# Kernel optimization log

Measured on AMD Instinct MI355X. Metric: run time of the kernel, lower is better.

Reference implementation:

```python
import jax, jax.numpy as jnp
import numpy as np

B, LQ, LK = 4, 2048, 2048
DQ, DK, DO = 1024, 1024, 1024


def setup_inputs() -> dict:
    key = jax.random.key(0)
    ks = jax.random.split(key, 9)
    s = 0.02
    return {
        "query_input": jax.random.normal(ks[0], (B, LQ, DQ), jnp.float32),
        "key_input": jax.random.normal(ks[1], (B, LK, DK), jnp.float32),
        "value_input": jax.random.normal(ks[2], (B, LK, DK), jnp.float32),
        "Wq": jax.random.normal(ks[3], (DQ, DO), jnp.float32) * s,
        "bq": jax.random.normal(ks[4], (DO,), jnp.float32) * s,
        "Wk": jax.random.normal(ks[5], (DK, DO), jnp.float32) * s,
        "bk": jax.random.normal(ks[6], (DO,), jnp.float32) * s,
        "Wv": jax.random.normal(ks[7], (DK, DO), jnp.float32) * s,
        "bv": jax.random.normal(ks[8], (DO,), jnp.float32) * s,
    }


def reference(query_input, key_input, value_input, Wq, bq, Wk, bk, Wv, bv):
    scale = jnp.asarray(DO, query_input.dtype) ** 0.5
    q = query_input @ Wq + bq              # [B, Lq, D]
    k = key_input @ Wk + bk                # [B, Lk, D]
    v = value_input @ Wv + bv              # [B, Lk, D]
    attn = jnp.einsum("bqd,bkd->bqk", q, k) / scale
    attn = jax.nn.softmax(attn, axis=-1)
    return jnp.einsum("bqk,bkd->bqd", attn, v)
```

## Files before the change

kernel.cpp:

```cpp
#include <hip/hip_runtime.h>

typedef _Float16 f16x8 __attribute__((ext_vector_type(8)));
typedef _Float16 f16x4 __attribute__((ext_vector_type(4)));
typedef float f32x4 __attribute__((ext_vector_type(4)));

__device__ __forceinline__ void lds_load16(const _Float16* g, _Float16* l) {
    __builtin_amdgcn_global_load_lds(
        (const __attribute__((address_space(1))) void*)g,
        (__attribute__((address_space(3))) void*)l,
        16, 0, 0);
}

template <int MODE>
__global__ __launch_bounds__(256, 2)
void gemm_core(const _Float16* A0, const _Float16* B0, void* C0, const float* b0,
               const _Float16* A1, const _Float16* B1, void* C1, const float* b1,
               const _Float16* A2, const _Float16* B2, void* C2, const float* b2,
               float* rowsum)
{
    constexpr int K   = (MODE == 5) ? 2048 : 1024;
    constexpr int LDA = (MODE == 5) ? 2048 : 1024;
    constexpr int LDB = (MODE == 5) ? 8192 : 1024;

    const int z = blockIdx.z;
    const int bx = blockIdx.x, by = blockIdx.y;

    __shared__ __align__(16) _Float16 As[2][256 * 32];
    __shared__ __align__(16) _Float16 Bs[2][128 * 32];

    const int t    = threadIdx.x;
    const int w    = t >> 6;
    const int lane = t & 63;
    const int ln   = lane & 15;
    const int kq   = lane >> 4;
    const int wm   = (w & 1) * 128;
    const int wn   = (w >> 1) * 64;

    const _Float16* A;
    const _Float16* B;
    size_t cbase = 0;
    int m0, n0;

    if (MODE == 0) {
        A = z == 0 ? A0 : z == 1 ? A1 : A2;
        B = z == 0 ? B0 : z == 1 ? B1 : B2;
        if (z == 2) { m0 = (by & 3) * 256; n0 = ((by >> 2) * 8 + bx) * 128; }
        else        { m0 = by * 256;       n0 = bx * 128; }
    } else if (MODE == 3) {
        A = A0 + (size_t)z * 2048 * 1024;
        B = B0 + (size_t)z * 2048 * 1024;
        cbase = (size_t)z * 2048 * 2048;
        rowsum += z * 2048;
        m0 = (by >> 1) * 256;
        n0 = ((by & 1) * 8 + bx) * 128;
    } else {
        A = A0 + (size_t)z * 2048 * 2048;
        B = B0 + (size_t)z * 2048;
        cbase = (size_t)z * 2048 * 1024;
        rowsum += z * 2048;
        m0 = by * 256;
        n0 = bx * 128;
    }

    const int r4 = t >> 2;
    const int sc = ((t & 3) ^ ((t >> 3) & 3)) * 8;
    const _Float16* gA = A + (size_t)(m0 + r4) * LDA + sc;
    const _Float16* gB = B + (size_t)(n0 + r4) * LDB + sc;

    auto stage = [&](int b, int k0) {
#pragma unroll
        for (int s = 0; s < 4; ++s)
            lds_load16(gA + k0 + (size_t)s * 64 * LDA, As[b] + s * 2048 + w * 512);
        lds_load16(gB + k0,                     Bs[b] + w * 512);
        lds_load16(gB + k0 + (size_t)64 * LDB,  Bs[b] + 2048 + w * 512);
    };

    const int swz   = (kq ^ ((ln >> 1) & 3)) * 8;
    const int abase = (wm + ln) * 32 + swz;
    const int bbase = (wn + ln) * 32 + swz;

    f32x4 acc[8][4] = {};

    stage(0, 0);
    int cur = 0;
#pragma unroll 2
    for (int k0 = 0; k0 < K; k0 += 32) {
        __syncthreads();
        if (k0 + 32 < K) stage(cur ^ 1, k0 + 32);
        const _Float16* Ab = As[cur] + abase;
        const _Float16* Bb = Bs[cur] + bbase;
        f16x8 af[8], bf[4];
#pragma unroll
        for (int i = 0; i < 8; ++i)
            af[i] = *(const f16x8*)(Ab + i * 512);
#pragma unroll
        for (int j = 0; j < 4; ++j)
            bf[j] = *(const f16x8*)(Bb + j * 512);
#pragma unroll
        for (int i = 0; i < 8; ++i)
#pragma unroll
            for (int j = 0; j < 4; ++j)
                acc[i][j] = __builtin_amdgcn_mfma_f32_16x16x32_f16(af[i], bf[j], acc[i][j], 0, 0, 0);
        cur ^= 1;
    }

    if (MODE == 0) {
        _Float16* Cp = (_Float16*)(z == 0 ? C0 : z == 1 ? C1 : C2);
        const float* bp = z == 0 ? b0 : z == 1 ? b1 : b2;
        const int ldc = (z == 2) ? 8192 : 1024;
#pragma unroll
        for (int i = 0; i < 8; ++i) {
            const int rbase = m0 + wm + i * 16 + kq * 4;
#pragma unroll
            for (int j = 0; j < 4; ++j) {
                const int gcol = n0 + wn + j * 16 + ln;
#pragma unroll
                for (int r = 0; r < 4; ++r) {
                    float vv = acc[i][j][r] + (z == 2 ? bp[rbase + r] : bp[gcol]);
                    Cp[(size_t)(rbase + r) * ldc + gcol] = (_Float16)vv;
                }
            }
        }
    } else if (MODE == 3) {
        _Float16* Ch = (_Float16*)C0;
#pragma unroll
        for (int i = 0; i < 8; ++i) {
            const int rbase = m0 + wm + i * 16 + kq * 4;
            float rs[4] = {0.f, 0.f, 0.f, 0.f};
#pragma unroll
            for (int j = 0; j < 4; ++j) {
                const int gcol = n0 + wn + j * 16 + ln;
#pragma unroll
                for (int r = 0; r < 4; ++r) {
                    float e = __expf(acc[i][j][r] * 0.03125f);
                    Ch[cbase + (size_t)(rbase + r) * 2048 + gcol] = (_Float16)e;
                    rs[r] += e;
                }
            }
#pragma unroll
            for (int r = 0; r < 4; ++r) {
                float s = rs[r];
                s += __shfl_xor(s, 1);
                s += __shfl_xor(s, 2);
                s += __shfl_xor(s, 4);
                s += __shfl_xor(s, 8);
                if (ln == 0) atomicAdd(&rowsum[rbase + r], s);
            }
        }
    } else {
        float* Cf = (float*)C0;
#pragma unroll
        for (int i = 0; i < 8; ++i) {
            const int rbase = m0 + wm + i * 16 + kq * 4;
            float inv[4];
#pragma unroll
            for (int r = 0; r < 4; ++r) inv[r] = 1.f / rowsum[rbase + r];
#pragma unroll
            for (int j = 0; j < 4; ++j) {
                const int gcol = n0 + wn + j * 16 + ln;
#pragma unroll
                for (int r = 0; r < 4; ++r)
                    Cf[cbase + (size_t)(rbase + r) * 1024 + gcol] = acc[i][j][r] * inv[r];
            }
        }
    }
}

__global__ __launch_bounds__(256)
void prep(const float4* __restrict__ x0, _Float16* __restrict__ y0,
          const float4* __restrict__ x1, _Float16* __restrict__ y1,
          const float4* __restrict__ x2, _Float16* __restrict__ y2,
          const float* __restrict__ W0, _Float16* __restrict__ T0,
          const float* __restrict__ W1, _Float16* __restrict__ T1,
          const float* __restrict__ W2, _Float16* __restrict__ T2,
          float* __restrict__ rowsum)
{
    if (blockIdx.y < 3) {
        const size_t i = (size_t)blockIdx.x * 256 + threadIdx.x;
        const float4* x = blockIdx.y == 0 ? x0 : blockIdx.y == 1 ? x1 : x2;
        _Float16*    yy = blockIdx.y == 0 ? y0 : blockIdx.y == 1 ? y1 : y2;
        float4 f = x[i];
        f16x4 o = { (_Float16)f.x, (_Float16)f.y, (_Float16)f.z, (_Float16)f.w };
        *(f16x4*)(yy + i * 4) = o;
        if (blockIdx.y == 0 && blockIdx.x < 32)
            rowsum[blockIdx.x * 256 + threadIdx.x] = 0.f;
        return;
    }
    if (blockIdx.x >= 3072) return;
    const int zz = blockIdx.x >> 10;
    const int tb = blockIdx.x & 1023;
    const float* W = zz == 0 ? W0 : zz == 1 ? W1 : W2;
    _Float16*   WT = zz == 0 ? T0 : zz == 1 ? T1 : T2;
    __shared__ float tile[32][33];
    const int bxs = (tb & 31) * 32;
    const int bys = (tb >> 5) * 32;
    const int tx = threadIdx.x & 31;
    const int ty = threadIdx.x >> 5;
#pragma unroll
    for (int i = ty; i < 32; i += 8)
        tile[i][tx] = W[(size_t)(bys + i) * 1024 + bxs + tx];
    __syncthreads();
#pragma unroll
    for (int i = ty; i < 32; i += 8)
        WT[(size_t)(bxs + i) * 1024 + bys + tx] = (_Float16)tile[tx][i];
}

extern "C" void kernel_launch(void* const* d_in, const int* in_sizes, int n_in,
                              void* d_out, int out_size, void* d_ws, size_t ws_size,
                              hipStream_t stream)
{
    const float* Xq = (const float*)d_in[0];
    const float* Xk = (const float*)d_in[1];
    const float* Xv = (const float*)d_in[2];
    const float* Wq = (const float*)d_in[3];
    const float* bq = (const float*)d_in[4];
    const float* Wk = (const float*)d_in[5];
    const float* bk = (const float*)d_in[6];
    const float* Wv = (const float*)d_in[7];
    const float* bv = (const float*)d_in[8];
    float* out = (float*)d_out;

    const size_t XN = (size_t)8192 * 1024;
    const size_t WN = (size_t)1024 * 1024;

    _Float16* ws  = (_Float16*)d_ws;
    _Float16* Xqh = ws;
    _Float16* Xkh = Xqh + XN;
    _Float16* Xvh = Xkh + XN;
    _Float16* WqT = Xvh + XN;
    _Float16* WkT = WqT + WN;
    _Float16* WvT = WkT + WN;
    _Float16* qh  = WvT + WN;
    _Float16* kh  = qh + XN;
    _Float16* vT  = kh + XN;
    _Float16* S   = vT + XN;
    float* rowsum = (float*)(S + (size_t)4 * 2048 * 2048);

    {
        dim3 g(8192, 4);
        prep<<<g, 256, 0, stream>>>((const float4*)Xq, Xqh,
                                    (const float4*)Xk, Xkh,
                                    (const float4*)Xv, Xvh,
                                    Wq, WqT, Wk, WkT, Wv, WvT, rowsum);
    }

    {
        dim3 g(8, 32, 3);
        gemm_core<0><<<g, 256, 0, stream>>>(
            Xqh, WqT, qh, bq,
            Xkh, WkT, kh, bk,
            WvT, Xvh, vT, bv,
            nullptr);
    }

    {
        dim3 g(8, 16, 4);
        gemm_core<3><<<g, 256, 0, stream>>>(
            qh, kh, S, nullptr,
            nullptr, nullptr, nullptr, nullptr,
            nullptr, nullptr, nullptr, nullptr,
            rowsum);
    }

    {
        dim3 g(8, 8, 4);
        gemm_core<5><<<g, 256, 0, stream>>>(
            S, vT, out, nullptr,
            nullptr, nullptr, nullptr, nullptr,
            nullptr, nullptr, nullptr, nullptr,
            rowsum);
    }
}
```

Measured before the change: 354.4 us.

## Rework GEMM core into 256x256 tiles with 8 waves and interleaved ping-pong pipeline

Grows the GEMM block tile from 256x128 with K=32 to 256x256 with K=64 and 512 threads (8 waves), and remaps block indices to match. The main loop becomes a hand-scheduled ping-pong: LDS loads of A and B fragments are interleaved with MFMA quarter-tiles, separated by explicit barriers, waitcnts and setprio, while the next K-tile is prefetched in pieces. The goal is more data reuse per block and better overlap of global loads, LDS reads and MFMAs. It raises LDS use to 128KB per block, which likely limits occupancy to one block per CU despite launch_bounds(512,2). Grids are halved, so fewer blocks cover the CUs, and the epilogue must stay consistent with the new per-wave layout.

```diff
diff --git a/kernel.cpp b/kernel.cpp
--- a/kernel.cpp
+++ b/kernel.cpp
@@ -12,7 +12,7 @@
 }
 
 template <int MODE>
-__global__ __launch_bounds__(256, 2)
+__global__ __launch_bounds__(512, 2)
 void gemm_core(const _Float16* A0, const _Float16* B0, void* C0, const float* b0,
                const _Float16* A1, const _Float16* B1, void* C1, const float* b1,
                const _Float16* A2, const _Float16* B2, void* C2, const float* b2,
@@ -21,20 +21,20 @@
     constexpr int K   = (MODE == 5) ? 2048 : 1024;
     constexpr int LDA = (MODE == 5) ? 2048 : 1024;
     constexpr int LDB = (MODE == 5) ? 8192 : 1024;
+    constexpr int NT  = K / 64;
+
+    __shared__ __align__(16) _Float16 As[2][256 * 64];
+    __shared__ __align__(16) _Float16 Bs[2][256 * 64];
 
     const int z = blockIdx.z;
     const int bx = blockIdx.x, by = blockIdx.y;
-
-    __shared__ __align__(16) _Float16 As[2][256 * 32];
-    __shared__ __align__(16) _Float16 Bs[2][128 * 32];
-
     const int t    = threadIdx.x;
     const int w    = t >> 6;
     const int lane = t & 63;
     const int ln   = lane & 15;
     const int kq   = lane >> 4;
-    const int wm   = (w & 1) * 128;
-    const int wn   = (w >> 1) * 64;
+    const int wm   = (w >> 2) * 128;
+    const int wn   = (w & 3) * 64;
 
     const _Float16* A;
     const _Float16* B;
@@ -44,64 +44,147 @@
     if (MODE == 0) {
         A = z == 0 ? A0 : z == 1 ? A1 : A2;
         B = z == 0 ? B0 : z == 1 ? B1 : B2;
-        if (z == 2) { m0 = (by & 3) * 256; n0 = ((by >> 2) * 8 + bx) * 128; }
-        else        { m0 = by * 256;       n0 = bx * 128; }
+        if (z == 2) { m0 = (by & 3) * 256;             n0 = (bx * 4 + (by >> 2)) * 256; }
+        else        { m0 = (bx * 4 + (by >> 2)) * 256; n0 = (by & 3) * 256; }
     } else if (MODE == 3) {
         A = A0 + (size_t)z * 2048 * 1024;
         B = B0 + (size_t)z * 2048 * 1024;
         cbase = (size_t)z * 2048 * 2048;
         rowsum += z * 2048;
-        m0 = (by >> 1) * 256;
-        n0 = ((by & 1) * 8 + bx) * 128;
+        m0 = ((bx & 3) * 2 + (by >> 2)) * 256;
+        n0 = ((bx >> 2) * 4 + (by & 3)) * 256;
     } else {
         A = A0 + (size_t)z * 2048 * 2048;
         B = B0 + (size_t)z * 2048;
         cbase = (size_t)z * 2048 * 1024;
         rowsum += z * 2048;
-        m0 = by * 256;
-        n0 = bx * 128;
-    }
-
-    const int r4 = t >> 2;
-    const int sc = ((t & 3) ^ ((t >> 3) & 3)) * 8;
-    const _Float16* gA = A + (size_t)(m0 + r4) * LDA + sc;
-    const _Float16* gB = B + (size_t)(n0 + r4) * LDB + sc;
-
-    auto stage = [&](int b, int k0) {
-#pragma unroll
-        for (int s = 0; s < 4; ++s)
-            lds_load16(gA + k0 + (size_t)s * 64 * LDA, As[b] + s * 2048 + w * 512);
-        lds_load16(gB + k0,                     Bs[b] + w * 512);
-        lds_load16(gB + k0 + (size_t)64 * LDB,  Bs[b] + 2048 + w * 512);
+        m0 = bx * 256;
+        n0 = by * 256;
+    }
+
+    const int l3 = lane >> 3;
+    const int lc = ((lane & 7) ^ l3) * 8;
+    const _Float16* gA = A + (size_t)(m0 + w * 16 + l3) * LDA + lc;
+    const _Float16* gB = B + (size_t)(n0 + w * 16 + l3) * LDB + lc;
+
+    auto stA = [&](int b, int kt, int h) {
+        const _Float16* g = gA + (size_t)(h * 128) * LDA + kt * 64;
+        _Float16* l = As[b] + h * 8192 + w * 1024;
+        lds_load16(g, l);
+        lds_load16(g + (size_t)8 * LDA, l + 512);
     };
-
-    const int swz   = (kq ^ ((ln >> 1) & 3)) * 8;
-    const int abase = (wm + ln) * 32 + swz;
-    const int bbase = (wn + ln) * 32 + swz;
-
+    auto stB = [&](int b, int kt, int h) {
+        const _Float16* g = gB + (size_t)(h * 128) * LDB + kt * 64;
+        _Float16* l = Bs[b] + h * 8192 + w * 1024;
+        lds_load16(g, l);
+        lds_load16(g + (size_t)8 * LDB, l + 512);
+    };
+
+    const int xr  = ln & 7;
+    const int sk0 = ((0 + kq) ^ xr) * 8;
+    const int sk1 = ((4 + kq) ^ xr) * 8;
+    const int ra  = (wm + ln) * 64;
+    const int rb  = (wn + ln) * 64;
+
+    f16x8 af[4][2], bf[4][2];
     f32x4 acc[8][4] = {};
 
-    stage(0, 0);
-    int cur = 0;
-#pragma unroll 2
-    for (int k0 = 0; k0 < K; k0 += 32) {
-        __syncthreads();
-        if (k0 + 32 < K) stage(cur ^ 1, k0 + 32);
-        const _Float16* Ab = As[cur] + abase;
-        const _Float16* Bb = Bs[cur] + bbase;
-        f16x8 af[8], bf[4];
-#pragma unroll
-        for (int i = 0; i < 8; ++i)
-            af[i] = *(const f16x8*)(Ab + i * 512);
-#pragma unroll
-        for (int j = 0; j < 4; ++j)
-            bf[j] = *(const f16x8*)(Bb + j * 512);
-#pragma unroll
-        for (int i = 0; i < 8; ++i)
-#pragma unroll
-            for (int j = 0; j < 4; ++j)
-                acc[i][j] = __builtin_amdgcn_mfma_f32_16x16x32_f16(af[i], bf[j], acc[i][j], 0, 0, 0);
-        cur ^= 1;
+    stA(0, 0, 0); stA(0, 0, 1); stB(0, 0, 0); stB(0, 0, 1);
+
+    for (int kt = 0; kt < NT; kt += 2) {
+#pragma unroll
+        for (int hlf = 0; hlf < 2; ++hlf) {
+            const int  b  = hlf;
+            const int  kc = kt + hlf;
+            const bool pf = (kc + 1 < NT);
+            const _Float16* Ab = As[b];
+            const _Float16* Bb = Bs[b];
+
+            if (pf) {
+                stA(b ^ 1, kc + 1, 0); stA(b ^ 1, kc + 1, 1);
+                asm volatile("s_waitcnt vmcnt(4)" ::: "memory");
+            } else {
+                asm volatile("s_waitcnt vmcnt(0)" ::: "memory");
+            }
+            __builtin_amdgcn_s_barrier();
+            __builtin_amdgcn_sched_barrier(0);
+#pragma unroll
+            for (int i = 0; i < 4; ++i) {
+                af[i][0] = *(const f16x8*)(Ab + ra + i * 1024 + sk0);
+                af[i][1] = *(const f16x8*)(Ab + ra + i * 1024 + sk1);
+            }
+#pragma unroll
+            for (int j = 0; j < 2; ++j) {
+                bf[j][0] = *(const f16x8*)(Bb + rb + j * 1024 + sk0);
+                bf[j][1] = *(const f16x8*)(Bb + rb + j * 1024 + sk1);
+            }
+            asm volatile("s_waitcnt lgkmcnt(0)" ::: "memory");
+            __builtin_amdgcn_sched_barrier(0);
+            __builtin_amdgcn_s_setprio(1);
+#pragma unroll
+            for (int i = 0; i < 4; ++i)
+#pragma unroll
+                for (int j = 0; j < 2; ++j) {
+                    acc[i][j] = __builtin_amdgcn_mfma_f32_16x16x32_f16(af[i][0], bf[j][0], acc[i][j], 0, 0, 0);
+                    acc[i][j] = __builtin_amdgcn_mfma_f32_16x16x32_f16(af[i][1], bf[j][1], acc[i][j], 0, 0, 0);
+                }
+            __builtin_amdgcn_s_setprio(0);
+            __builtin_amdgcn_s_barrier();
+            __builtin_amdgcn_sched_barrier(0);
+
+#pragma unroll
+            for (int j = 2; j < 4; ++j) {
+                bf[j][0] = *(const f16x8*)(Bb + rb + j * 1024 + sk0);
+                bf[j][1] = *(const f16x8*)(Bb + rb + j * 1024 + sk1);
+            }
+            if (pf) { stB(b ^ 1, kc + 1, 0); stB(b ^ 1, kc + 1, 1); }
+            __builtin_amdgcn_s_barrier();
+            asm volatile("s_waitcnt lgkmcnt(0)" ::: "memory");
+            __builtin_amdgcn_sched_barrier(0);
+            __builtin_amdgcn_s_setprio(1);
+#pragma unroll
+            for (int i = 0; i < 4; ++i)
+#pragma unroll
+                for (int j = 2; j < 4; ++j) {
+                    acc[i][j] = __builtin_amdgcn_mfma_f32_16x16x32_f16(af[i][0], bf[j][0], acc[i][j], 0, 0, 0);
+                    acc[i][j] = __builtin_amdgcn_mfma_f32_16x16x32_f16(af[i][1], bf[j][1], acc[i][j], 0, 0, 0);
+                }
+            __builtin_amdgcn_s_setprio(0);
+            __builtin_amdgcn_s_barrier();
+            __builtin_amdgcn_sched_barrier(0);
+
+#pragma unroll
+            for (int i = 0; i < 4; ++i) {
+                af[i][0] = *(const f16x8*)(Ab + ra + (i + 4) * 1024 + sk0);
+                af[i][1] = *(const f16x8*)(Ab + ra + (i + 4) * 1024 + sk1);
+            }
+            __builtin_amdgcn_s_barrier();
+            asm volatile("s_waitcnt lgkmcnt(0)" ::: "memory");
+            __builtin_amdgcn_sched_barrier(0);
+            __builtin_amdgcn_s_setprio(1);
+#pragma unroll
+            for (int i = 0; i < 4; ++i)
+#pragma unroll
+                for (int j = 0; j < 2; ++j) {
+                    acc[i + 4][j] = __builtin_amdgcn_mfma_f32_16x16x32_f16(af[i][0], bf[j][0], acc[i + 4][j], 0, 0, 0);
+                    acc[i + 4][j] = __builtin_amdgcn_mfma_f32_16x16x32_f16(af[i][1], bf[j][1], acc[i + 4][j], 0, 0, 0);
+                }
+            __builtin_amdgcn_s_setprio(0);
+            __builtin_amdgcn_s_barrier();
+            __builtin_amdgcn_sched_barrier(0);
+
+            __builtin_amdgcn_s_setprio(1);
+#pragma unroll
+            for (int i = 0; i < 4; ++i)
+#pragma unroll
+                for (int j = 2; j < 4; ++j) {
+                    acc[i + 4][j] = __builtin_amdgcn_mfma_f32_16x16x32_f16(af[i][0], bf[j][0], acc[i + 4][j], 0, 0, 0);
+                    acc[i + 4][j] = __builtin_amdgcn_mfma_f32_16x16x32_f16(af[i][1], bf[j][1], acc[i + 4][j], 0, 0, 0);
+                }
+            __builtin_amdgcn_s_setprio(0);
+            __builtin_amdgcn_s_barrier();
+            __builtin_amdgcn_sched_barrier(0);
+        }
     }
 
     if (MODE == 0) {
@@ -245,8 +328,8 @@
     }
 
     {
-        dim3 g(8, 32, 3);
-        gemm_core<0><<<g, 256, 0, stream>>>(
+        dim3 g(8, 16, 3);
+        gemm_core<0><<<g, 512, 0, stream>>>(
             Xqh, WqT, qh, bq,
             Xkh, WkT, kh, bk,
             WvT, Xvh, vT, bv,
@@ -254,8 +337,8 @@
     }
 
     {
-        dim3 g(8, 16, 4);
-        gemm_core<3><<<g, 256, 0, stream>>>(
+        dim3 g(8, 8, 4);
+        gemm_core<3><<<g, 512, 0, stream>>>(
             qh, kh, S, nullptr,
             nullptr, nullptr, nullptr, nullptr,
             nullptr, nullptr, nullptr, nullptr,
@@ -263,8 +346,8 @@
     }
 
     {
-        dim3 g(8, 8, 4);
-        gemm_core<5><<<g, 256, 0, stream>>>(
+        dim3 g(8, 4, 4);
+        gemm_core<5><<<g, 512, 0, stream>>>(
             S, vT, out, nullptr,
             nullptr, nullptr, nullptr, nullptr,
             nullptr, nullptr, nullptr, nullptr,
```

Measured after the change: 341.5 us. 1.04x faster.

## Shrink GEMM tile to 128x128 with triple-buffered LDS pipeline and inline ds_reads

Applied to the files above, without the earlier changes.

Reduces the block tile from 256x128 to 128x128, doubling grid sizes, and raises the occupancy hint to 3 blocks per CU. The LDS pipeline becomes three stages with prefetch two tiles ahead, explicit vmcnt/lgkmcnt waits, raw s_barrier, and sched_barrier fences. Fragment loads use inline-asm ds_read_b128 with immediate offsets, and MFMA blocks run at raised wave priority. Block-to-tile mapping is remapped for L2 locality. This aims to overlap global loads with compute and improve occupancy, at the cost of less register-level reuse per tile and more blocks.

```diff
diff --git a/kernel.cpp b/kernel.cpp
--- a/kernel.cpp
+++ b/kernel.cpp
@@ -3,6 +3,7 @@
 typedef _Float16 f16x8 __attribute__((ext_vector_type(8)));
 typedef _Float16 f16x4 __attribute__((ext_vector_type(4)));
 typedef float f32x4 __attribute__((ext_vector_type(4)));
+typedef int   v4i   __attribute__((ext_vector_type(4)));
 
 __device__ __forceinline__ void lds_load16(const _Float16* g, _Float16* l) {
     __builtin_amdgcn_global_load_lds(
@@ -11,8 +12,18 @@
         16, 0, 0);
 }
 
+template <int OFF>
+__device__ __forceinline__ f16x8 ldsrO(unsigned a) {
+    v4i r;
+    if constexpr (OFF == 0)
+        asm volatile("ds_read_b128 %0, %1" : "=v"(r) : "v"(a));
+    else
+        asm volatile("ds_read_b128 %0, %1 offset:%2" : "=v"(r) : "v"(a), "i"(OFF));
+    return __builtin_bit_cast(f16x8, r);
+}
+
 template <int MODE>
-__global__ __launch_bounds__(256, 2)
+__global__ __launch_bounds__(256, 3)
 void gemm_core(const _Float16* A0, const _Float16* B0, void* C0, const float* b0,
                const _Float16* A1, const _Float16* B1, void* C1, const float* b1,
                const _Float16* A2, const _Float16* B2, void* C2, const float* b2,
@@ -21,44 +32,44 @@
     constexpr int K   = (MODE == 5) ? 2048 : 1024;
     constexpr int LDA = (MODE == 5) ? 2048 : 1024;
     constexpr int LDB = (MODE == 5) ? 8192 : 1024;
-
-    const int z = blockIdx.z;
+    constexpr int NT  = K / 32;
+
+    __shared__ __align__(16) _Float16 As[3][128 * 32];
+    __shared__ __align__(16) _Float16 Bs[3][128 * 32];
+
+    const int z_ = blockIdx.z;
     const int bx = blockIdx.x, by = blockIdx.y;
-
-    __shared__ __align__(16) _Float16 As[2][256 * 32];
-    __shared__ __align__(16) _Float16 Bs[2][128 * 32];
-
     const int t    = threadIdx.x;
     const int w    = t >> 6;
     const int lane = t & 63;
     const int ln   = lane & 15;
     const int kq   = lane >> 4;
-    const int wm   = (w & 1) * 128;
+    const int wm   = (w & 1) * 64;
     const int wn   = (w >> 1) * 64;
 
     const _Float16* A;
     const _Float16* B;
     size_t cbase = 0;
-    int m0, n0;
+    int m0, n0, z = z_;
 
     if (MODE == 0) {
         A = z == 0 ? A0 : z == 1 ? A1 : A2;
         B = z == 0 ? B0 : z == 1 ? B1 : B2;
-        if (z == 2) { m0 = (by & 3) * 256; n0 = ((by >> 2) * 8 + bx) * 128; }
-        else        { m0 = by * 256;       n0 = bx * 128; }
+        if (z == 2) { m0 = (by & 7) * 128; n0 = (bx * 8 + (by >> 3)) * 128; }
+        else        { m0 = (bx * 8 + (by >> 3)) * 128; n0 = (by & 7) * 128; }
     } else if (MODE == 3) {
         A = A0 + (size_t)z * 2048 * 1024;
         B = B0 + (size_t)z * 2048 * 1024;
         cbase = (size_t)z * 2048 * 2048;
         rowsum += z * 2048;
-        m0 = (by >> 1) * 256;
-        n0 = ((by & 1) * 8 + bx) * 128;
+        m0 = (bx * 2 + (by >> 4)) * 128;
+        n0 = (by & 15) * 128;
     } else {
         A = A0 + (size_t)z * 2048 * 2048;
         B = B0 + (size_t)z * 2048;
         cbase = (size_t)z * 2048 * 1024;
         rowsum += z * 2048;
-        m0 = by * 256;
+        m0 = by * 128;
         n0 = bx * 128;
     }
 
@@ -66,42 +77,63 @@
     const int sc = ((t & 3) ^ ((t >> 3) & 3)) * 8;
     const _Float16* gA = A + (size_t)(m0 + r4) * LDA + sc;
     const _Float16* gB = B + (size_t)(n0 + r4) * LDB + sc;
-
-    auto stage = [&](int b, int k0) {
-#pragma unroll
-        for (int s = 0; s < 4; ++s)
-            lds_load16(gA + k0 + (size_t)s * 64 * LDA, As[b] + s * 2048 + w * 512);
-        lds_load16(gB + k0,                     Bs[b] + w * 512);
-        lds_load16(gB + k0 + (size_t)64 * LDB,  Bs[b] + 2048 + w * 512);
+    _Float16* const lA = &As[0][0] + w * 512;
+    _Float16* const lB = &Bs[0][0] + w * 512;
+
+    auto stage = [&](unsigned bufE, int kt) {
+        lds_load16(gA + kt * 32,                     lA + bufE);
+        lds_load16(gA + (size_t)64 * LDA + kt * 32,  lA + bufE + 2048);
+        lds_load16(gB + kt * 32,                     lB + bufE);
+        lds_load16(gB + (size_t)64 * LDB + kt * 32,  lB + bufE + 2048);
     };
 
-    const int swz   = (kq ^ ((ln >> 1) & 3)) * 8;
-    const int abase = (wm + ln) * 32 + swz;
-    const int bbase = (wn + ln) * 32 + swz;
-
-    f32x4 acc[8][4] = {};
+    const int sk = (kq ^ ((ln >> 1) & 3)) * 16;
+    const unsigned uA0 = (unsigned)(uintptr_t)(__attribute__((address_space(3))) _Float16*)&As[0][0];
+    const unsigned uB0 = (unsigned)(uintptr_t)(__attribute__((address_space(3))) _Float16*)&Bs[0][0];
+    const unsigned vAbase = uA0 + (wm + ln) * 64 + sk;
+    const unsigned vBbase = uB0 + (wn + ln) * 64 + sk;
+
+    f32x4 acc[4][4] = {};
 
     stage(0, 0);
-    int cur = 0;
-#pragma unroll 2
-    for (int k0 = 0; k0 < K; k0 += 32) {
-        __syncthreads();
-        if (k0 + 32 < K) stage(cur ^ 1, k0 + 32);
-        const _Float16* Ab = As[cur] + abase;
-        const _Float16* Bb = Bs[cur] + bbase;
-        f16x8 af[8], bf[4];
-#pragma unroll
-        for (int i = 0; i < 8; ++i)
-            af[i] = *(const f16x8*)(Ab + i * 512);
-#pragma unroll
-        for (int j = 0; j < 4; ++j)
-            bf[j] = *(const f16x8*)(Bb + j * 512);
-#pragma unroll
-        for (int i = 0; i < 8; ++i)
+    stage(4096, 1);
+    asm volatile("s_waitcnt vmcnt(4)" ::: "memory");
+    __builtin_amdgcn_s_barrier();
+    __builtin_amdgcn_sched_barrier(0);
+
+    unsigned offR = 0;
+    unsigned offW = 8192;
+
+    for (int kc = 0; kc < NT; ++kc) {
+        const unsigned aA = vAbase + offR;
+        const unsigned aB = vBbase + offR;
+        f16x8 af[4], bf[4];
+        af[0] = ldsrO<0>(aA);    af[1] = ldsrO<1024>(aA);
+        af[2] = ldsrO<2048>(aA); af[3] = ldsrO<3072>(aA);
+        bf[0] = ldsrO<0>(aB);    bf[1] = ldsrO<1024>(aB);
+        bf[2] = ldsrO<2048>(aB); bf[3] = ldsrO<3072>(aB);
+
+        const bool pf = (kc + 2 < NT);
+        if (pf) stage(offW, kc + 2);
+
+        asm volatile("s_waitcnt lgkmcnt(0)" ::: "memory");
+        __builtin_amdgcn_sched_barrier(0);
+        __builtin_amdgcn_s_setprio(1);
+#pragma unroll
+        for (int i = 0; i < 4; ++i)
 #pragma unroll
             for (int j = 0; j < 4; ++j)
                 acc[i][j] = __builtin_amdgcn_mfma_f32_16x16x32_f16(af[i], bf[j], acc[i][j], 0, 0, 0);
-        cur ^= 1;
+        __builtin_amdgcn_s_setprio(0);
+        __builtin_amdgcn_sched_barrier(0);
+
+        if (pf) asm volatile("s_waitcnt vmcnt(4)" ::: "memory");
+        else    asm volatile("s_waitcnt vmcnt(0)" ::: "memory");
+        __builtin_amdgcn_s_barrier();
+        __builtin_amdgcn_sched_barrier(0);
+
+        offR = (offR == 16384u) ? 0u : offR + 8192u;
+        offW = (offW == 8192u)  ? 0u : offW + 4096u;
     }
 
     if (MODE == 0) {
@@ -109,7 +141,7 @@
         const float* bp = z == 0 ? b0 : z == 1 ? b1 : b2;
         const int ldc = (z == 2) ? 8192 : 1024;
 #pragma unroll
-        for (int i = 0; i < 8; ++i) {
+        for (int i = 0; i < 4; ++i) {
             const int rbase = m0 + wm + i * 16 + kq * 4;
 #pragma unroll
             for (int j = 0; j < 4; ++j) {
@@ -124,7 +156,7 @@
     } else if (MODE == 3) {
         _Float16* Ch = (_Float16*)C0;
 #pragma unroll
-        for (int i = 0; i < 8; ++i) {
+        for (int i = 0; i < 4; ++i) {
             const int rbase = m0 + wm + i * 16 + kq * 4;
             float rs[4] = {0.f, 0.f, 0.f, 0.f};
 #pragma unroll
@@ -150,7 +182,7 @@
     } else {
         float* Cf = (float*)C0;
 #pragma unroll
-        for (int i = 0; i < 8; ++i) {
+        for (int i = 0; i < 4; ++i) {
             const int rbase = m0 + wm + i * 16 + kq * 4;
             float inv[4];
 #pragma unroll
@@ -245,7 +277,7 @@
     }
 
     {
-        dim3 g(8, 32, 3);
+        dim3 g(8, 64, 3);
         gemm_core<0><<<g, 256, 0, stream>>>(
             Xqh, WqT, qh, bq,
             Xkh, WkT, kh, bk,
@@ -254,7 +286,7 @@
     }
 
     {
-        dim3 g(8, 16, 4);
+        dim3 g(8, 32, 4);
         gemm_core<3><<<g, 256, 0, stream>>>(
             qh, kh, S, nullptr,
             nullptr, nullptr, nullptr, nullptr,
@@ -263,7 +295,7 @@
     }
 
     {
-        dim3 g(8, 8, 4);
+        dim3 g(8, 16, 4);
         gemm_core<5><<<g, 256, 0, stream>>>(
             S, vT, out, nullptr,
             nullptr, nullptr, nullptr, nullptr,
```

Measured after the change: 317.3 us. 10.5% less time.
